# Optimization experiments

Hardware: AMD Instinct MI355X
Metric: run time of the kernel (lower is better)

## Reference

```python
import jax, jax.numpy as jnp
import numpy as np

N = 200000
E = 3200000
NHID = 128
NUM_GRAPHS = 512


def setup_inputs() -> dict:
    key = jax.random.key(0)
    k_x, k_ei, k_b, k_n, k_w1, k_w2, k_bl = jax.random.split(key, 7)
    x = jax.random.normal(k_x, (N, NHID), dtype=jnp.float32)
    edge_index = jax.random.randint(k_ei, (2, E), 0, N, dtype=jnp.int32)
    batch = jnp.sort(jax.random.randint(k_b, (N,), 0, NUM_GRAPHS, dtype=jnp.int32))
    noise = jax.random.normal(k_n, (N, NHID), dtype=jnp.float32)
    # Generator params (xavier-ish init)
    h = NHID // 2
    W1 = jax.random.normal(k_w1, (NHID, h), dtype=jnp.float32) * np.float32(1.0 / np.sqrt(NHID))
    b1 = jnp.zeros((h,), dtype=jnp.float32)
    W2 = jax.random.normal(k_w2, (h, NHID), dtype=jnp.float32) * np.float32(1.0 / np.sqrt(h))
    b2 = jnp.zeros((NHID,), dtype=jnp.float32)
    return {"x": x, "edge_index": edge_index, "batch": batch, "noise": noise,
            "W1": W1, "b1": b1, "W2": W2, "b2": b2}


def scatter_mean(src_feats, dst_idx, num_nodes):
    # sum messages per destination node, then divide by in-degree (clamped to 1)
    summed = jax.ops.segment_sum(src_feats, dst_idx, num_segments=num_nodes)
    counts = jax.ops.segment_sum(jnp.ones((src_feats.shape[0],), src_feats.dtype),
                                 dst_idx, num_segments=num_nodes)
    return summed / jnp.maximum(counts, 1.0)[:, None]


def reference(x, edge_index, batch, noise, W1, b1, W2, b2):
    src, dst = edge_index[0], edge_index[1]
    # NeighborPropagate: mean aggregation of x_j = x[src] at dst
    x_neighbor = scatter_mean(x[src], dst, x.shape[0])  # [N, nhid]
    g = x_neighbor + noise
    # Generator MLP: relu(fc2(relu(fc1(g))))
    h = jax.nn.relu(g @ W1 + b1)
    x_gen = jax.nn.relu(h @ W2 + b2)
    return x_gen
```

## Files before the change

kernel.cpp:

```cpp
#include <hip/hip_runtime.h>

#define NHID 128
#define HDIM 64
#define EPB 8192
#define MAXBKT 1024
#define CAP 6144

typedef __attribute__((ext_vector_type(8))) short bf16x8;
typedef __attribute__((ext_vector_type(4))) float f32x4;

__device__ __forceinline__ unsigned short f2bf_rn(float f) {
    union { float f; unsigned u; } c; c.f = f;
    unsigned r = c.u + 0x7fffu + ((c.u >> 16) & 1u);
    return (unsigned short)(r >> 16);
}
__device__ __forceinline__ float bf_lo(unsigned d) {
    union { unsigned u; float f; } c; c.u = d << 16; return c.f;
}
__device__ __forceinline__ float bf_hi(unsigned d) {
    union { unsigned u; float f; } c; c.u = d & 0xFFFF0000u; return c.f;
}

__global__ __launch_bounds__(256) void prep_bf16(const float* __restrict__ x,
                                                 unsigned short* __restrict__ xh,
                                                 long long total8) {
    long long t = (long long)blockIdx.x * blockDim.x + threadIdx.x;
    if (t >= total8) return;
    const float4 a = *(const float4*)(x + t * 8);
    const float4 b = *(const float4*)(x + t * 8 + 4);
    ushort4 p, q;
    p.x = f2bf_rn(a.x); p.y = f2bf_rn(a.y); p.z = f2bf_rn(a.z); p.w = f2bf_rn(a.w);
    q.x = f2bf_rn(b.x); q.y = f2bf_rn(b.y); q.z = f2bf_rn(b.z); q.w = f2bf_rn(b.w);
    *(ushort4*)(xh + t * 8) = p;
    *(ushort4*)(xh + t * 8 + 4) = q;
}

__global__ __launch_bounds__(256) void bucket_scatter(const int* __restrict__ src,
                                                      const int* __restrict__ dst,
                                                      int* __restrict__ bucket_cursor,
                                                      unsigned int* __restrict__ bpack,
                                                      int E, int NBKT) {
    __shared__ int h[MAXBKT];
    __shared__ int lofs[MAXBKT];
    __shared__ int lcur[MAXBKT];
    __shared__ unsigned sbuf[EPB];
    int t = threadIdx.x;
    long long base = (long long)blockIdx.x * EPB;
    int rem = (int)(E - base);
    int nev = rem < EPB ? rem : EPB;

    for (int i = t; i < MAXBKT; i += 256) h[i] = 0;
    __syncthreads();

    for (int p = 0; p < EPB / 256; ++p) {
        int e = p * 256 + t;
        if (e < nev) atomicAdd(&h[((unsigned)dst[base + e]) >> 8], 1);
    }
    __syncthreads();

    #pragma unroll
    for (int j = 0; j < 4; ++j) lofs[t + j * 256] = h[t + j * 256];
    __syncthreads();
    for (int off = 1; off < MAXBKT; off <<= 1) {
        int v0, v1, v2, v3;
        {
            int i0 = t, i1 = t + 256, i2 = t + 512, i3 = t + 768;
            v0 = lofs[i0] + (i0 >= off ? lofs[i0 - off] : 0);
            v1 = lofs[i1] + (i1 >= off ? lofs[i1 - off] : 0);
            v2 = lofs[i2] + (i2 >= off ? lofs[i2 - off] : 0);
            v3 = lofs[i3] + (i3 >= off ? lofs[i3 - off] : 0);
        }
        __syncthreads();
        lofs[t] = v0; lofs[t + 256] = v1; lofs[t + 512] = v2; lofs[t + 768] = v3;
        __syncthreads();
    }

    for (int i = t; i < MAXBKT; i += 256) {
        int c = h[i];
        lcur[i] = lofs[i] - c;
        h[i] = c ? (i * CAP + atomicAdd(&bucket_cursor[i], c)) : 0;
    }
    __syncthreads();

    for (int p = 0; p < EPB / 256; ++p) {
        int e = p * 256 + t;
        if (e < nev) {
            int d = dst[base + e];
            int s = src[base + e];
            int b = ((unsigned)d) >> 8;
            int pos = atomicAdd(&lcur[b], 1);
            sbuf[pos] = (((unsigned)d & 255u) << 24) | (unsigned)s;
        }
    }
    __syncthreads();

    for (int p = 0; p < EPB / 256; ++p) {
        int j = p * 256 + t;
        if (j < nev) {
            int lo = 0, hi = NBKT - 1;
            while (lo < hi) {
                int mid = (lo + hi) >> 1;
                if (lofs[mid] > j) hi = mid; else lo = mid + 1;
            }
            int b = lo;
            int prev = b ? lofs[b - 1] : 0;
            int gpos = h[b] + (j - prev);
            if (gpos < (b + 1) * CAP)
                bpack[gpos] = sbuf[j];
        }
    }
}

__global__ __launch_bounds__(256) void bucket_build(unsigned int* __restrict__ bpack,
                                                    const int* __restrict__ bucket_cursor,
                                                    int* __restrict__ cnt,
                                                    int* __restrict__ rowptr,
                                                    int N) {
    __shared__ unsigned ebuf[CAP];
    __shared__ int lc[256];
    __shared__ int sc[256];
    int b = blockIdx.x, t = threadIdx.x;
    int beg = b * CAP;
    int m = bucket_cursor[b]; if (m > CAP) m = CAP;
    lc[t] = 0;
    __syncthreads();
    for (int i = t; i < m; i += 256) {
        unsigned v = bpack[beg + i];
        ebuf[i] = v;
        atomicAdd(&lc[v >> 24], 1);
    }
    __syncthreads();
    int myc = lc[t];
    sc[t] = myc; __syncthreads();
    for (int off = 1; off < 256; off <<= 1) {
        int v = (t >= off) ? sc[t - off] : 0;
        __syncthreads();
        sc[t] += v;
        __syncthreads();
    }
    int excl = sc[t] - myc;
    int node = b * 256 + t;
    if (node < N) { cnt[node] = myc; rowptr[node] = beg + excl; }
    lc[t] = excl;
    __syncthreads();
    for (int i = t; i < m; i += 256) {
        unsigned v = ebuf[i];
        int pos = atomicAdd(&lc[v >> 24], 1);
        bpack[beg + pos] = v & 0xFFFFFFu;
    }
}

__global__ __launch_bounds__(256) void gather_fuse(
    const unsigned short* __restrict__ xh, const unsigned int* __restrict__ perm,
    const int* __restrict__ rowptr, const int* __restrict__ cnt,
    const float* __restrict__ noise, unsigned short* __restrict__ g, int N)
{
    long long t = (long long)blockIdx.x * blockDim.x + threadIdx.x;
    int n = (int)(t >> 4);
    int c = (int)(t & 15);
    if (n >= N) return;
    int beg = rowptr[n];
    int deg = cnt[n];
    float a0 = 0.f, a1 = 0.f, a2 = 0.f, a3 = 0.f, a4 = 0.f, a5 = 0.f, a6 = 0.f, a7 = 0.f;
    const unsigned short* xb = xh + c * 8;
    int i = 0;
    for (; i + 3 < deg; i += 4) {
        unsigned s0 = perm[beg + i];
        unsigned s1 = perm[beg + i + 1];
        unsigned s2 = perm[beg + i + 2];
        unsigned s3 = perm[beg + i + 3];
        uint4 u0 = *(const uint4*)(xb + (long long)s0 * NHID);
        uint4 u1 = *(const uint4*)(xb + (long long)s1 * NHID);
        uint4 u2 = *(const uint4*)(xb + (long long)s2 * NHID);
        uint4 u3 = *(const uint4*)(xb + (long long)s3 * NHID);
        a0 += (bf_lo(u0.x) + bf_lo(u1.x)) + (bf_lo(u2.x) + bf_lo(u3.x));
        a1 += (bf_hi(u0.x) + bf_hi(u1.x)) + (bf_hi(u2.x) + bf_hi(u3.x));
        a2 += (bf_lo(u0.y) + bf_lo(u1.y)) + (bf_lo(u2.y) + bf_lo(u3.y));
        a3 += (bf_hi(u0.y) + bf_hi(u1.y)) + (bf_hi(u2.y) + bf_hi(u3.y));
        a4 += (bf_lo(u0.z) + bf_lo(u1.z)) + (bf_lo(u2.z) + bf_lo(u3.z));
        a5 += (bf_hi(u0.z) + bf_hi(u1.z)) + (bf_hi(u2.z) + bf_hi(u3.z));
        a6 += (bf_lo(u0.w) + bf_lo(u1.w)) + (bf_lo(u2.w) + bf_lo(u3.w));
        a7 += (bf_hi(u0.w) + bf_hi(u1.w)) + (bf_hi(u2.w) + bf_hi(u3.w));
    }
    for (; i < deg; ++i) {
        unsigned s0 = perm[beg + i];
        uint4 u = *(const uint4*)(xb + (long long)s0 * NHID);
        a0 += bf_lo(u.x); a1 += bf_hi(u.x);
        a2 += bf_lo(u.y); a3 += bf_hi(u.y);
        a4 += bf_lo(u.z); a5 += bf_hi(u.z);
        a6 += bf_lo(u.w); a7 += bf_hi(u.w);
    }
    float inv = 1.0f / fmaxf((float)deg, 1.0f);
    const float* nr = noise + (long long)n * NHID + c * 8;
    float4 n0 = *(const float4*)nr;
    float4 n1 = *(const float4*)(nr + 4);
    ushort4 p, q;
    p.x = f2bf_rn(fmaf(a0, inv, n0.x));
    p.y = f2bf_rn(fmaf(a1, inv, n0.y));
    p.z = f2bf_rn(fmaf(a2, inv, n0.z));
    p.w = f2bf_rn(fmaf(a3, inv, n0.w));
    q.x = f2bf_rn(fmaf(a4, inv, n1.x));
    q.y = f2bf_rn(fmaf(a5, inv, n1.y));
    q.z = f2bf_rn(fmaf(a6, inv, n1.z));
    q.w = f2bf_rn(fmaf(a7, inv, n1.w));
    unsigned short* go = g + (long long)n * 256 + c * 8;
    *(ushort4*)go = p;
    *(ushort4*)(go + 4) = q;
}

__global__ __launch_bounds__(256) void mlp_mfma(
    float* out,
    const float* __restrict__ W1, const float* __restrict__ b1,
    const float* __restrict__ W2, const float* __restrict__ b2,
    int N)
{
    __shared__ __align__(16) unsigned short w1t[64 * 136];
    __shared__ __align__(16) unsigned short w2t[128 * 72];
    __shared__ __align__(16) unsigned short ht[4][16 * 72];
    __shared__ float b1s[HDIM];
    __shared__ float b2s[NHID];

    int t = threadIdx.x;
    int wave = t >> 6;
    int lane = t & 63;
    int m = lane & 15;
    int quad = lane >> 4;

    #pragma unroll 4
    for (int p = 0; p < 32; ++p) {
        int idx = p * 256 + t;
        int k = idx >> 6, n = idx & 63;
        w1t[n * 136 + k] = f2bf_rn(W1[idx]);
    }
    #pragma unroll 4
    for (int p = 0; p < 32; ++p) {
        int idx = p * 256 + t;
        int k = idx >> 7, n = idx & 127;
        w2t[n * 72 + k] = f2bf_rn(W2[idx]);
    }
    if (t < HDIM) b1s[t] = b1[t];
    else if (t < HDIM + NHID) b2s[t - HDIM] = b2[t - HDIM];
    __syncthreads();

    int node = blockIdx.x * 64 + wave * 16 + m;
    int nodec = node < N ? node : N - 1;

    const unsigned short* grow = (const unsigned short*)out + (long long)nodec * 256;
    bf16x8 afrag[4];
    #pragma unroll
    for (int kc = 0; kc < 4; ++kc)
        afrag[kc] = *(const bf16x8*)(grow + kc * 32 + quad * 8);

    unsigned short* hw = &ht[wave][0];
    #pragma unroll
    for (int nt = 0; nt < 4; ++nt) {
        f32x4 acc = {0.f, 0.f, 0.f, 0.f};
        #pragma unroll
        for (int kc = 0; kc < 4; ++kc) {
            bf16x8 bfrag = *(const bf16x8*)&w1t[(nt * 16 + m) * 136 + kc * 32 + quad * 8];
            acc = __builtin_amdgcn_mfma_f32_16x16x32_bf16(afrag[kc], bfrag, acc, 0, 0, 0);
        }
        float bb = b1s[nt * 16 + m];
        #pragma unroll
        for (int r = 0; r < 4; ++r) {
            hw[(quad * 4 + r) * 72 + nt * 16 + m] = f2bf_rn(fmaxf(acc[r] + bb, 0.0f));
        }
    }

    bf16x8 a2[2];
    #pragma unroll
    for (int kc = 0; kc < 2; ++kc)
        a2[kc] = *(const bf16x8*)&hw[m * 72 + kc * 32 + quad * 8];

    float* obase = out + ((long long)blockIdx.x * 64 + wave * 16) * NHID;
    #pragma unroll
    for (int nt = 0; nt < 8; ++nt) {
        f32x4 acc = {0.f, 0.f, 0.f, 0.f};
        #pragma unroll
        for (int kc = 0; kc < 2; ++kc) {
            bf16x8 bfrag = *(const bf16x8*)&w2t[(nt * 16 + m) * 72 + kc * 32 + quad * 8];
            acc = __builtin_amdgcn_mfma_f32_16x16x32_bf16(a2[kc], bfrag, acc, 0, 0, 0);
        }
        float bb = b2s[nt * 16 + m];
        #pragma unroll
        for (int r = 0; r < 4; ++r) {
            int orow = blockIdx.x * 64 + wave * 16 + quad * 4 + r;
            if (orow < N)
                obase[(quad * 4 + r) * NHID + nt * 16 + m] = fmaxf(acc[r] + bb, 0.0f);
        }
    }
}

extern "C" void kernel_launch(void* const* d_in, const int* in_sizes, int n_in,
                              void* d_out, int out_size, void* d_ws, size_t ws_size,
                              hipStream_t stream) {
    const float* x     = (const float*)d_in[0];
    const int*   ei    = (const int*)d_in[1];
    const float* noise = (const float*)d_in[3];
    const float* W1    = (const float*)d_in[4];
    const float* b1    = (const float*)d_in[5];
    const float* W2    = (const float*)d_in[6];
    const float* b2    = (const float*)d_in[7];
    float* out = (float*)d_out;

    const int N = in_sizes[2];
    const int E = in_sizes[1] / 2;
    const int* src = ei;
    const int* dst = ei + E;
    const int NBKT = (N + 255) >> 8;

    int* bucket_cursor = (int*)d_ws;
    int* cnt           = bucket_cursor + MAXBKT;
    int* rowptr        = cnt + N;
    unsigned int* bpack = (unsigned int*)(rowptr + N);
    unsigned short* xh  = (unsigned short*)(bpack + (size_t)NBKT * CAP);

    hipMemsetAsync(bucket_cursor, 0, (size_t)MAXBKT * sizeof(int), stream);

    {
        long long total8 = (long long)N * NHID / 8;
        prep_bf16<<<(int)((total8 + 255) / 256), 256, 0, stream>>>(x, xh, total8);
    }
    {
        const int EB = (int)(((long long)E + EPB - 1) / EPB);
        bucket_scatter<<<EB, 256, 0, stream>>>(src, dst, bucket_cursor, bpack, E, NBKT);
    }
    bucket_build<<<NBKT, 256, 0, stream>>>(bpack, bucket_cursor, cnt, rowptr, N);
    {
        long long total = (long long)N * 16;
        gather_fuse<<<(int)((total + 255) / 256), 256, 0, stream>>>(
            xh, bpack, rowptr, cnt, noise, (unsigned short*)out, N);
    }
    mlp_mfma<<<(N + 63) / 64, 256, 0, stream>>>(out, W1, b1, W2, b2, N);
}
```

Before: 480.6 us.

## Replace atomic bucket cursors with deterministic histogram-scan scatter and deeper gather unroll

Bucket scatter now computes per-block histograms first (fused with the bf16 conversion of x into one launch), scans them per bucket and across buckets, and writes edges to deterministic, compactly packed offsets. This removes the global atomic cursors, the fixed-capacity bucket slots and the memset. The gather loop also gains an 8-way unrolled path so more neighbour loads are in flight at once. The cost is two extra small scan kernels, a second pass over dst, and a per-block histogram matrix in workspace.

Result: slower. 490.9 us (+2.1%).

```diff
diff --git a/kernel.cpp b/kernel.cpp
--- a/kernel.cpp
+++ b/kernel.cpp
@@ -21,25 +21,81 @@
     union { unsigned u; float f; } c; c.u = d & 0xFFFF0000u; return c.f;
 }
 
-__global__ __launch_bounds__(256) void prep_bf16(const float* __restrict__ x,
-                                                 unsigned short* __restrict__ xh,
-                                                 long long total8) {
-    long long t = (long long)blockIdx.x * blockDim.x + threadIdx.x;
-    if (t >= total8) return;
-    const float4 a = *(const float4*)(x + t * 8);
-    const float4 b = *(const float4*)(x + t * 8 + 4);
-    ushort4 p, q;
-    p.x = f2bf_rn(a.x); p.y = f2bf_rn(a.y); p.z = f2bf_rn(a.z); p.w = f2bf_rn(a.w);
-    q.x = f2bf_rn(b.x); q.y = f2bf_rn(b.y); q.z = f2bf_rn(b.z); q.w = f2bf_rn(b.w);
-    *(ushort4*)(xh + t * 8) = p;
-    *(ushort4*)(xh + t * 8 + 4) = q;
-}
-
-__global__ __launch_bounds__(256) void bucket_scatter(const int* __restrict__ src,
-                                                      const int* __restrict__ dst,
-                                                      int* __restrict__ bucket_cursor,
-                                                      unsigned int* __restrict__ bpack,
-                                                      int E, int NBKT) {
+__global__ __launch_bounds__(256) void hist_prep(
+    const int* __restrict__ dst, int* __restrict__ hmat,
+    const float* __restrict__ x, unsigned short* __restrict__ xh,
+    int E, int EB, long long total8)
+{
+    if ((int)blockIdx.x < EB) {
+        __shared__ int h[MAXBKT];
+        int t = threadIdx.x;
+        for (int i = t; i < MAXBKT; i += 256) h[i] = 0;
+        __syncthreads();
+        long long base = (long long)blockIdx.x * EPB;
+        for (int p = 0; p < EPB / 256; ++p) {
+            long long e = base + p * 256 + t;
+            if (e < E) atomicAdd(&h[((unsigned)dst[e]) >> 8], 1);
+        }
+        __syncthreads();
+        int* outp = hmat + (size_t)blockIdx.x * MAXBKT;
+        for (int i = t; i < MAXBKT; i += 256) outp[i] = h[i];
+    } else {
+        long long t8 = (long long)((int)blockIdx.x - EB) * 256 + threadIdx.x;
+        if (t8 >= total8) return;
+        const float4 a = *(const float4*)(x + t8 * 8);
+        const float4 b = *(const float4*)(x + t8 * 8 + 4);
+        ushort4 p, q;
+        p.x = f2bf_rn(a.x); p.y = f2bf_rn(a.y); p.z = f2bf_rn(a.z); p.w = f2bf_rn(a.w);
+        q.x = f2bf_rn(b.x); q.y = f2bf_rn(b.y); q.z = f2bf_rn(b.z); q.w = f2bf_rn(b.w);
+        *(ushort4*)(xh + t8 * 8) = p;
+        *(ushort4*)(xh + t8 * 8 + 4) = q;
+    }
+}
+
+__global__ __launch_bounds__(256) void scan_blocks(int* __restrict__ hmat,
+                                                   int* __restrict__ btot,
+                                                   int EB) {
+    __shared__ int sc[512];
+    int j = blockIdx.x;
+    int t = threadIdx.x;
+    int i1 = t, i2 = t + 256;
+    int o1 = (i1 < EB) ? hmat[(size_t)i1 * MAXBKT + j] : 0;
+    int o2 = (i2 < EB) ? hmat[(size_t)i2 * MAXBKT + j] : 0;
+    sc[i1] = o1; sc[i2] = o2;
+    __syncthreads();
+    for (int off = 1; off < 512; off <<= 1) {
+        int v1 = (i1 >= off) ? sc[i1 - off] : 0;
+        int v2 = (i2 >= off) ? sc[i2 - off] : 0;
+        __syncthreads();
+        sc[i1] += v1; sc[i2] += v2;
+        __syncthreads();
+    }
+    if (i1 < EB) hmat[(size_t)i1 * MAXBKT + j] = sc[i1] - o1;
+    if (i2 < EB) hmat[(size_t)i2 * MAXBKT + j] = sc[i2] - o2;
+    if (t == 0) btot[j] = sc[511];
+}
+
+__global__ __launch_bounds__(1024) void scan_bbase(const int* __restrict__ btot,
+                                                   int* __restrict__ bbase, int NBKT) {
+    __shared__ int sc[1024];
+    int t = threadIdx.x;
+    int v = (t < NBKT) ? btot[t] : 0;
+    sc[t] = v;
+    __syncthreads();
+    for (int off = 1; off < 1024; off <<= 1) {
+        int u = (t >= off) ? sc[t - off] : 0;
+        __syncthreads();
+        sc[t] += u;
+        __syncthreads();
+    }
+    bbase[t] = sc[t] - v;
+}
+
+__global__ __launch_bounds__(256) void scatter_det(
+    const int* __restrict__ src, const int* __restrict__ dst,
+    const int* __restrict__ hmat, const int* __restrict__ bbase,
+    unsigned int* __restrict__ bpack, int E, int NBKT)
+{
     __shared__ int h[MAXBKT];
     __shared__ int lofs[MAXBKT];
     __shared__ int lcur[MAXBKT];
@@ -51,37 +107,31 @@
 
     for (int i = t; i < MAXBKT; i += 256) h[i] = 0;
     __syncthreads();
-
     for (int p = 0; p < EPB / 256; ++p) {
         int e = p * 256 + t;
         if (e < nev) atomicAdd(&h[((unsigned)dst[base + e]) >> 8], 1);
     }
     __syncthreads();
-
     #pragma unroll
-    for (int j = 0; j < 4; ++j) lofs[t + j * 256] = h[t + j * 256];
+    for (int j2 = 0; j2 < 4; ++j2) lofs[t + j2 * 256] = h[t + j2 * 256];
     __syncthreads();
     for (int off = 1; off < MAXBKT; off <<= 1) {
-        int v0, v1, v2, v3;
-        {
-            int i0 = t, i1 = t + 256, i2 = t + 512, i3 = t + 768;
-            v0 = lofs[i0] + (i0 >= off ? lofs[i0 - off] : 0);
-            v1 = lofs[i1] + (i1 >= off ? lofs[i1 - off] : 0);
-            v2 = lofs[i2] + (i2 >= off ? lofs[i2 - off] : 0);
-            v3 = lofs[i3] + (i3 >= off ? lofs[i3 - off] : 0);
-        }
-        __syncthreads();
-        lofs[t] = v0; lofs[t + 256] = v1; lofs[t + 512] = v2; lofs[t + 768] = v3;
-        __syncthreads();
-    }
-
+        int i0 = t, i1 = t + 256, i2 = t + 512, i3 = t + 768;
+        int v0 = lofs[i0] + (i0 >= off ? lofs[i0 - off] : 0);
+        int v1 = lofs[i1] + (i1 >= off ? lofs[i1 - off] : 0);
+        int v2 = lofs[i2] + (i2 >= off ? lofs[i2 - off] : 0);
+        int v3 = lofs[i3] + (i3 >= off ? lofs[i3 - off] : 0);
+        __syncthreads();
+        lofs[i0] = v0; lofs[i1] = v1; lofs[i2] = v2; lofs[i3] = v3;
+        __syncthreads();
+    }
+    const int* lst = hmat + (size_t)blockIdx.x * MAXBKT;
     for (int i = t; i < MAXBKT; i += 256) {
         int c = h[i];
         lcur[i] = lofs[i] - c;
-        h[i] = c ? (i * CAP + atomicAdd(&bucket_cursor[i], c)) : 0;
-    }
-    __syncthreads();
-
+        h[i] = bbase[i] + lst[i];
+    }
+    __syncthreads();
     for (int p = 0; p < EPB / 256; ++p) {
         int e = p * 256 + t;
         if (e < nev) {
@@ -93,7 +143,6 @@
         }
     }
     __syncthreads();
-
     for (int p = 0; p < EPB / 256; ++p) {
         int j = p * 256 + t;
         if (j < nev) {
@@ -104,15 +153,14 @@
             }
             int b = lo;
             int prev = b ? lofs[b - 1] : 0;
-            int gpos = h[b] + (j - prev);
-            if (gpos < (b + 1) * CAP)
-                bpack[gpos] = sbuf[j];
+            bpack[h[b] + (j - prev)] = sbuf[j];
         }
     }
 }
 
 __global__ __launch_bounds__(256) void bucket_build(unsigned int* __restrict__ bpack,
-                                                    const int* __restrict__ bucket_cursor,
+                                                    const int* __restrict__ bbase,
+                                                    const int* __restrict__ btot,
                                                     int* __restrict__ cnt,
                                                     int* __restrict__ rowptr,
                                                     int N) {
@@ -120,8 +168,8 @@
     __shared__ int lc[256];
     __shared__ int sc[256];
     int b = blockIdx.x, t = threadIdx.x;
-    int beg = b * CAP;
-    int m = bucket_cursor[b]; if (m > CAP) m = CAP;
+    int beg = bbase[b];
+    int m = btot[b]; if (m > CAP) m = CAP;
     lc[t] = 0;
     __syncthreads();
     for (int i = t; i < m; i += 256) {
@@ -164,6 +212,40 @@
     float a0 = 0.f, a1 = 0.f, a2 = 0.f, a3 = 0.f, a4 = 0.f, a5 = 0.f, a6 = 0.f, a7 = 0.f;
     const unsigned short* xb = xh + c * 8;
     int i = 0;
+    for (; i + 7 < deg; i += 8) {
+        unsigned s0 = perm[beg + i];
+        unsigned s1 = perm[beg + i + 1];
+        unsigned s2 = perm[beg + i + 2];
+        unsigned s3 = perm[beg + i + 3];
+        unsigned s4 = perm[beg + i + 4];
+        unsigned s5 = perm[beg + i + 5];
+        unsigned s6 = perm[beg + i + 6];
+        unsigned s7 = perm[beg + i + 7];
+        uint4 u0 = *(const uint4*)(xb + (long long)s0 * NHID);
+        uint4 u1 = *(const uint4*)(xb + (long long)s1 * NHID);
+        uint4 u2 = *(const uint4*)(xb + (long long)s2 * NHID);
+        uint4 u3 = *(const uint4*)(xb + (long long)s3 * NHID);
+        uint4 u4 = *(const uint4*)(xb + (long long)s4 * NHID);
+        uint4 u5 = *(const uint4*)(xb + (long long)s5 * NHID);
+        uint4 u6 = *(const uint4*)(xb + (long long)s6 * NHID);
+        uint4 u7 = *(const uint4*)(xb + (long long)s7 * NHID);
+        a0 += ((bf_lo(u0.x) + bf_lo(u1.x)) + (bf_lo(u2.x) + bf_lo(u3.x)))
+            + ((bf_lo(u4.x) + bf_lo(u5.x)) + (bf_lo(u6.x) + bf_lo(u7.x)));
+        a1 += ((bf_hi(u0.x) + bf_hi(u1.x)) + (bf_hi(u2.x) + bf_hi(u3.x)))
+            + ((bf_hi(u4.x) + bf_hi(u5.x)) + (bf_hi(u6.x) + bf_hi(u7.x)));
+        a2 += ((bf_lo(u0.y) + bf_lo(u1.y)) + (bf_lo(u2.y) + bf_lo(u3.y)))
+            + ((bf_lo(u4.y) + bf_lo(u5.y)) + (bf_lo(u6.y) + bf_lo(u7.y)));
+        a3 += ((bf_hi(u0.y) + bf_hi(u1.y)) + (bf_hi(u2.y) + bf_hi(u3.y)))
+            + ((bf_hi(u4.y) + bf_hi(u5.y)) + (bf_hi(u6.y) + bf_hi(u7.y)));
+        a4 += ((bf_lo(u0.z) + bf_lo(u1.z)) + (bf_lo(u2.z) + bf_lo(u3.z)))
+            + ((bf_lo(u4.z) + bf_lo(u5.z)) + (bf_lo(u6.z) + bf_lo(u7.z)));
+        a5 += ((bf_hi(u0.z) + bf_hi(u1.z)) + (bf_hi(u2.z) + bf_hi(u3.z)))
+            + ((bf_hi(u4.z) + bf_hi(u5.z)) + (bf_hi(u6.z) + bf_hi(u7.z)));
+        a6 += ((bf_lo(u0.w) + bf_lo(u1.w)) + (bf_lo(u2.w) + bf_lo(u3.w)))
+            + ((bf_lo(u4.w) + bf_lo(u5.w)) + (bf_lo(u6.w) + bf_lo(u7.w)));
+        a7 += ((bf_hi(u0.w) + bf_hi(u1.w)) + (bf_hi(u2.w) + bf_hi(u3.w)))
+            + ((bf_hi(u4.w) + bf_hi(u5.w)) + (bf_hi(u6.w) + bf_hi(u7.w)));
+    }
     for (; i + 3 < deg; i += 4) {
         unsigned s0 = perm[beg + i];
         unsigned s1 = perm[beg + i + 1];
@@ -308,24 +390,23 @@
     const int* src = ei;
     const int* dst = ei + E;
     const int NBKT = (N + 255) >> 8;
-
-    int* bucket_cursor = (int*)d_ws;
-    int* cnt           = bucket_cursor + MAXBKT;
-    int* rowptr        = cnt + N;
+    const int EB = (int)(((long long)E + EPB - 1) / EPB);
+
+    int* hmat           = (int*)d_ws;
+    int* btot           = hmat + (size_t)EB * MAXBKT;
+    int* bbase          = btot + MAXBKT;
+    int* cnt            = bbase + MAXBKT;
+    int* rowptr         = cnt + N;
     unsigned int* bpack = (unsigned int*)(rowptr + N);
-    unsigned short* xh  = (unsigned short*)(bpack + (size_t)NBKT * CAP);
-
-    hipMemsetAsync(bucket_cursor, 0, (size_t)MAXBKT * sizeof(int), stream);
-
-    {
-        long long total8 = (long long)N * NHID / 8;
-        prep_bf16<<<(int)((total8 + 255) / 256), 256, 0, stream>>>(x, xh, total8);
-    }
-    {
-        const int EB = (int)(((long long)E + EPB - 1) / EPB);
-        bucket_scatter<<<EB, 256, 0, stream>>>(src, dst, bucket_cursor, bpack, E, NBKT);
-    }
-    bucket_build<<<NBKT, 256, 0, stream>>>(bpack, bucket_cursor, cnt, rowptr, N);
+    unsigned short* xh  = (unsigned short*)(bpack + (size_t)E);
+
+    long long total8 = (long long)N * NHID / 8;
+    int prepB = (int)((total8 + 255) / 256);
+    hist_prep<<<EB + prepB, 256, 0, stream>>>(dst, hmat, x, xh, E, EB, total8);
+    scan_blocks<<<NBKT, 256, 0, stream>>>(hmat, btot, EB);
+    scan_bbase<<<1, 1024, 0, stream>>>(btot, bbase, NBKT);
+    scatter_det<<<EB, 256, 0, stream>>>(src, dst, hmat, bbase, bpack, E, NBKT);
+    bucket_build<<<NBKT, 256, 0, stream>>>(bpack, bbase, btot, cnt, rowptr, N);
     {
         long long total = (long long)N * 16;
         gather_fuse<<<(int)((total + 255) / 256), 256, 0, stream>>>(
```
